# Performance work log

Hardware: AMD Instinct MI355X
Metric: run time of the kernel (lower is better)

## Reference

```python
import jax, jax.numpy as jnp
import numpy as np

P, N, M, B = 5, 30000, 50000, 256
T, C, L, ED, H, EMB, TD, NL = 13, 16, 3, 4, 128, 64, 5, 3
SRC = jnp.repeat(jnp.arange(P), P)  # edge type i = src*P + dst
DST = jnp.tile(jnp.arange(P), P)


def _affine(x, W, b):
    # x: [P, n, i], W: [P, i, o], b: [P, o]
    return jnp.einsum('pni,pio->pno', x, W) + b[:, None, :]


def _lrelu(x, s=0.01):
    return jnp.where(x >= 0, x, s * x)


def _gat(h, W, a_s, a_d, We, a_e, b, edge_index, edge_attr):
    # h: [P, N, H]; per-edge-type GATConv (heads=1, no self loops) then hetero 'max' aggregation
    hs, hd = h[SRC], h[DST]                       # [25, N, H]
    xl = jnp.einsum('enh,ehf->enf', hs, W)        # transformed source features
    xr = jnp.einsum('enh,ehf->enf', hd, W)
    als = jnp.einsum('enf,ef->en', xl, a_s)
    ald = jnp.einsum('enf,ef->en', xr, a_d)

    def per_type(xl_e, als_e, ald_e, ea, We_e, ae_e, ei):
        src, dst = ei[0], ei[1]
        alpha = als_e[src] + ald_e[dst] + (ea @ We_e) @ ae_e
        alpha = jnp.where(alpha >= 0, alpha, 0.2 * alpha)  # GAT negative_slope=0.2
        amax = jax.ops.segment_max(alpha, dst, num_segments=N)
        ex = jnp.exp(alpha - amax[dst])
        den = jax.ops.segment_sum(ex, dst, num_segments=N)
        w = ex / (den[dst] + 1e-16)
        return jax.ops.segment_sum(w[:, None] * xl_e[src], dst, num_segments=N)

    out = jax.vmap(per_type)(xl, als, ald, edge_attr, We, a_e, edge_index)
    out = out + b[:, None, :]
    return out.reshape(P, P, N, H).max(axis=0)  # HeteroConv aggr='max' over source types


def setup_inputs():
    key = jax.random.key(0)
    ks = iter(jax.random.split(key, 64))
    def nrm(shape, s=1.0):
        return jax.random.normal(next(ks), shape, dtype=jnp.float32) * s
    w = 0.05
    inp = {
        'x': nrm((P, N, T)),
        'cond_x': nrm((P, N, C + L)),
        'edge_attr': nrm((P * P, M, ED)),
        'timesteps': jax.random.uniform(next(ks), (B,), dtype=jnp.float32),
        'te1_W': nrm((1, TD), w), 'te1_b': nrm((TD,), w),
        'te2_W': nrm((TD, TD), w), 'te2_b': nrm((TD,), w),
        'emb_W': nrm((P, T + L, EMB), w), 'emb_b': nrm((P, EMB), w),
        'cemb_W': nrm((P, C, EMB), w), 'cemb_b': nrm((P, EMB), w),
        'pa_W': nrm((P, 2 * EMB, 2 * EMB), w), 'pa_b': nrm((P, 2 * EMB), w),
        'pc_W': nrm((P, 2 * EMB, EMB), w), 'pc_b': nrm((P, EMB), w),
        'sl0_W': nrm((P, EMB + TD, H), w), 'sl0_b': nrm((P, H), w),
        'sl12_W': nrm((2, P, H + TD, H), w), 'sl12_b': nrm((2, P, H), w),
        'slout_W': nrm((P, H + TD, T), w), 'slout_b': nrm((P, T), w),
        'gat_W': nrm((NL, P * P, H, H), w), 'gat_as': nrm((NL, P * P, H), w),
        'gat_ad': nrm((NL, P * P, H), w), 'gat_We': nrm((NL, P * P, ED, H), w),
        'gat_ae': nrm((NL, P * P, H), w), 'gat_b': nrm((NL, P * P, H), w),
        'xc_W': nrm((NL, P, H, H // 2), w), 'xc_b': nrm((NL, P, H // 2), w),
        'cc_W': nrm((NL, P, H, H // 2), w), 'cc_b': nrm((NL, P, H // 2), w),
        'ca_W': nrm((NL, P, H, H), w), 'ca_b': nrm((NL, P, H), w),
        'batch_idx': jax.random.randint(next(ks), (P, N), 0, B),
        'edge_index': jax.random.randint(next(ks), (P * P, 2, M), 0, N),
    }
    return inp


def reference(x, cond_x, edge_attr, timesteps, te1_W, te1_b, te2_W, te2_b,
              emb_W, emb_b, cemb_W, cemb_b, pa_W, pa_b, pc_W, pc_b,
              sl0_W, sl0_b, sl12_W, sl12_b, slout_W, slout_b,
              gat_W, gat_as, gat_ad, gat_We, gat_ae, gat_b,
              xc_W, xc_b, cc_W, cc_b, ca_W, ca_b, batch_idx, edge_index):
    # time embedding: Linear(1,TD) -> SiLU -> Linear(TD,TD)
    temb = jax.nn.silu(timesteps[:, None] @ te1_W + te1_b) @ te2_W + te2_b  # [B, TD]
    cond, latent = cond_x[..., :C], cond_x[..., C:]
    h = _affine(jnp.concatenate([x, latent], -1), emb_W, emb_b)            # [P,N,EMB]
    ce = _affine(cond, cemb_W, cemb_b)
    h = jnp.concatenate([h, ce], -1)                                       # [P,N,2EMB]
    h = jax.nn.sigmoid(_affine(h, pa_W, pa_b)) * h                         # attention pooling
    h = _affine(h, pc_W, pc_b)                                             # [P,N,EMB]
    nt = temb[batch_idx]                                                   # [P,N,TD]
    h = jnp.concatenate([h, nt], -1)
    for l in range(NL):
        if l > 0:
            h = jnp.concatenate([h, nt], -1)
        Wl, bl = (sl0_W, sl0_b) if l == 0 else (sl12_W[l - 1], sl12_b[l - 1])
        h = _lrelu(_affine(h, Wl, bl))                                     # [P,N,H]
        comm = _lrelu(_gat(h, gat_W[l], gat_as[l], gat_ad[l], gat_We[l], gat_ae[l], gat_b[l], edge_index, edge_attr))
        h = jnp.concatenate([_affine(h, xc_W[l], xc_b[l]), _affine(comm, cc_W[l], cc_b[l])], -1)
        h = h + jax.nn.sigmoid(_affine(h, ca_W[l], ca_b[l])) * h
    h = jnp.concatenate([h, nt], -1)
    return _affine(h, slout_W, slout_b)                                    # [P,N,T]
```

## Files before the change

### kernel.cpp

```cpp
#include <hip/hip_runtime.h>
#include <cstdio>

using bf8 = __attribute__((ext_vector_type(8))) short;
using f4v = __attribute__((ext_vector_type(4))) float;
typedef unsigned short u16;
typedef unsigned int u32;

#define DEV __device__ __forceinline__

DEV float bf2f(u16 u){ return __uint_as_float(((u32)u) << 16); }
DEV u16 f2bf(float f){ u32 u = __float_as_uint(f); return (u16)((u + 0x7fffu + ((u >> 16) & 1u)) >> 16); }
DEV float sigm(float v){ return 1.f / (1.f + __expf(-v)); }

constexpr int P5 = 5, NN = 30000, MM = 50000, NE = 25, BB = 256;
constexpr int KC = 96;
constexpr int RS = KC * 2 + 16;
constexpr int RSA = 272;

__global__ void temb_k(const float* ts, const float* w1, const float* b1,
                       const float* w2, const float* b2, float* temb){
  int i = blockIdx.x * blockDim.x + threadIdx.x;
  if (i >= BB) return;
  float t = ts[i]; float z[5];
#pragma unroll
  for (int j = 0; j < 5; ++j){ float u = t * w1[j] + b1[j]; z[j] = u * sigm(u); }
#pragma unroll
  for (int j2 = 0; j2 < 5; ++j2){
    float s = b2[j2];
#pragma unroll
    for (int j = 0; j < 5; ++j) s += z[j] * w2[j * 5 + j2];
    temb[i * 5 + j2] = s;
  }
}

__global__ void wtransE_k(const float* __restrict__ W, u16* __restrict__ Wt,
                          int Kreal, int Kpad, int Nreal, int Nalloc, int total){
  int idx = blockIdx.x * blockDim.x + threadIdx.x;
  if (idx >= total) return;
  int k = idx % Kpad;
  int t2 = idx / Kpad;
  int f = t2 % Nalloc;
  int b = t2 / Nalloc;
  float v = (k < Kreal && f < Nreal) ? W[((size_t)b * Kreal + k) * Nreal + f] : 0.f;
  Wt[idx] = f2bf(v);
}

__global__ void embw_k(const float* emb_W, const float* emb_b, const float* cemb_W, const float* cemb_b,
                       u16* Wc, float* bc){
  int b = blockIdx.x, f = threadIdx.x;
  for (int k = 0; k < 32; ++k){
    float v = 0.f;
    if (f < 64){ if (k < 16) v = emb_W[((size_t)b * 16 + k) * 64 + f]; }
    else       { if (k >= 16) v = cemb_W[((size_t)b * 16 + (k - 16)) * 64 + (f - 64)]; }
    Wc[((size_t)b * 128 + f) * 32 + k] = f2bf(v);
  }
  bc[b * 128 + f] = (f < 64) ? emb_b[b * 64 + f] : cemb_b[b * 64 + (f - 64)];
}

__global__ void gwtT_k(const float* __restrict__ gW, u16* __restrict__ gWt){
  int idx = blockIdx.x * blockDim.x + threadIdx.x;
  if (idx >= 75 * 128 * 128) return;
  int h = idx & 127, f = (idx >> 7) & 127, le = idx >> 14;
  gWt[idx] = f2bf(gW[(size_t)le * 16384 + h * 128 + f]);
}

__global__ void gatred_k(const float* gW, const float* gas, const float* gad,
                         const float* gWe, const float* gae,
                         float* wswd, float* eaw){
  int le = blockIdx.x; int h = threadIdx.x;
  const float* W = gW + (size_t)le * 16384;
  const float* as_ = gas + le * 128;
  const float* ad_ = gad + le * 128;
  float wsv = 0.f, wdv = 0.f;
  for (int f = 0; f < 128; ++f){
    float w = W[h * 128 + f];
    wsv += w * as_[f]; wdv += w * ad_[f];
  }
  wswd[le * 256 + h] = wsv;
  wswd[le * 256 + 128 + h] = wdv;
  if (h < 4){
    const float* We = gWe + (size_t)le * 512;
    const float* ae = gae + le * 128;
    float s = 0.f;
    for (int f = 0; f < 128; ++f) s += We[h * 128 + f] * ae[f];
    eaw[le * 4 + h] = s;
  }
}

__global__ void abuild_k(const float* x, const float* cx, u16* A0){
  int idx = blockIdx.x * blockDim.x + threadIdx.x;
  if (idx >= P5 * NN) return;
  const float* xr = x + (size_t)idx * 13;
  const float* cr = cx + (size_t)idx * 19;
  u16* a0 = A0 + (size_t)idx * 32;
#pragma unroll
  for (int i = 0; i < 13; ++i) a0[i] = f2bf(xr[i]);
#pragma unroll
  for (int i = 0; i < 3; ++i) a0[13 + i] = f2bf(cr[16 + i]);
#pragma unroll
  for (int i = 0; i < 16; ++i) a0[16 + i] = f2bf(cr[i]);
}

__global__ void ntfill_k(u16* buf, int pitch, int co, const int* bidx, const float* temb){
  int idx = blockIdx.x * blockDim.x + threadIdx.x;
  if (idx >= P5 * NN) return;
  int b = bidx[idx];
  u16* r = buf + (size_t)idx * pitch;
#pragma unroll
  for (int j = 0; j < 5; ++j) r[co + j] = f2bf(temb[b * 5 + j]);
  for (int j = co + 5; j < pitch; ++j) r[j] = 0;
}

__global__ __launch_bounds__(1024) void csr_build_k(const int* __restrict__ EI, int* __restrict__ off,
                                                    int* __restrict__ srcC, int* __restrict__ minv){
  extern __shared__ int cntl[];
  __shared__ int wsum[16];
  int e = blockIdx.x, tid = threadIdx.x;
  int lane = tid & 63, wv = tid >> 6;
  for (int i = tid; i < NN; i += 1024) cntl[i] = 0;
  __syncthreads();
  const int* srcp = EI + (size_t)e * 2 * MM;
  const int* dstp = srcp + MM;
  for (int m = tid; m < MM; m += 1024) atomicAdd(&cntl[dstp[m]], 1);
  __syncthreads();
  int t0 = tid * 30, t1 = t0 + 30;
  if (t0 > NN) t0 = NN;
  if (t1 > NN) t1 = NN;
  int tsum = 0;
  for (int i = t0; i < t1; ++i) tsum += cntl[i];
  int s = tsum;
#pragma unroll
  for (int o = 1; o < 64; o <<= 1){ int t = __shfl_up(s, o, 64); if (lane >= o) s += t; }
  if (lane == 63) wsum[wv] = s;
  __syncthreads();
  if (wv == 0 && lane < 16){
    int t = wsum[lane];
#pragma unroll
    for (int o = 1; o < 16; o <<= 1){ int u = __shfl_up(t, o, 64); if (lane >= o) t += u; }
    wsum[lane] = t;
  }
  __syncthreads();
  int run = ((wv > 0) ? wsum[wv - 1] : 0) + (s - tsum);
  for (int i = t0; i < t1; ++i){
    int v = cntl[i];
    off[(size_t)e * (NN + 1) + i] = run;
    cntl[i] = run;
    run += v;
  }
  if (tid == 0) off[(size_t)e * (NN + 1) + NN] = wsum[15];
  __syncthreads();
  for (int m = tid; m < MM; m += 1024){
    int d = dstp[m];
    int pos = atomicAdd(&cntl[d], 1);
    srcC[(size_t)e * MM + pos] = srcp[m];
    minv[(size_t)e * MM + pos] = m;
  }
}

__global__ void eadot_k(const float* __restrict__ ea, const float* __restrict__ eaw,
                        const int* __restrict__ minv, float* __restrict__ eadot){
  int idx = blockIdx.x * blockDim.x + threadIdx.x;
  if (idx >= 3 * NE * MM) return;
  int l = idx / (NE * MM);
  int rem = idx - l * NE * MM;
  int e = rem / MM, pos = rem - e * MM;
  int m = minv[(size_t)e * MM + pos];
  const float* a4 = ea + ((size_t)e * MM + m) * 4;
  const float* ew = eaw + (size_t)(l * NE + e) * 4;
  eadot[idx] = a4[0] * ew[0] + a4[1] * ew[1] + a4[2] * ew[2] + a4[3] * ew[3];
}

__global__ __launch_bounds__(256) void dots2_k(const u16* __restrict__ hS, const float* __restrict__ wswd_l,
                                               float* __restrict__ als, float* __restrict__ ald){
  __shared__ u32 hl[64][65];
  __shared__ float wsl[10][129];
  int p = blockIdx.y;
  int n0 = blockIdx.x * 64;
  int tid = threadIdx.x;
  for (int i = tid; i < 10 * 128; i += 256){
    int col = i >> 7, k = i & 127;
    int e = (col < 5) ? (p * 5 + col) : ((col - 5) * 5 + p);
    wsl[col][k] = wswd_l[e * 256 + ((col < 5) ? 0 : 128) + k];
  }
  for (int i = tid; i < 64 * 64; i += 256){
    int r = i >> 6, kp = i & 63;
    int n = n0 + r;
    hl[r][kp] = (n < NN) ? ((const u32*)hS)[((size_t)p * NN + n) * 64 + kp] : 0u;
  }
  __syncthreads();
  int col = tid & 15, rbase = tid >> 4;
  if (col < 10){
#pragma unroll
    for (int pass = 0; pass < 4; ++pass){
      int r = rbase + pass * 16;
      int n = n0 + r;
      if (n >= NN) continue;
      float s = 0.f;
#pragma unroll
      for (int kp = 0; kp < 64; ++kp){
        u32 pr = hl[r][kp];
        s += bf2f((u16)(pr & 0xffffu)) * wsl[col][2 * kp]
           + bf2f((u16)(pr >> 16)) * wsl[col][2 * kp + 1];
      }
      if (col < 5) als[(size_t)(p * 5 + col) * NN + n] = s;
      else         ald[(size_t)((col - 5) * 5 + p) * NN + n] = s;
    }
  }
}

__global__ __launch_bounds__(256) void aexp_k(const float* __restrict__ als, const float* __restrict__ ald,
                                              const float* __restrict__ eadot_l, const int* __restrict__ srcC,
                                              const int* __restrict__ off, uint2* __restrict__ prec){
  int idx = blockIdx.x * blockDim.x + threadIdx.x;
  if (idx >= NE * NN) return;
  int e = idx / NN;
  int ro = off[(size_t)e + idx], re = off[(size_t)e + idx + 1];
  if (ro >= re) return;
  float av = ald[idx];
  const int* sc = srcC + (size_t)e * MM;
  const float* ed = eadot_l + (size_t)e * MM;
  const float* ale = als + (size_t)e * NN;
  float mx = -3.0e38f;
  for (int j = ro; j < re; ++j){
    float a = ale[sc[j]] + av + ed[j];
    a = (a >= 0.f) ? a : 0.2f * a;
    mx = fmaxf(mx, a);
  }
  for (int j = ro; j < re; ++j){
    int src = sc[j];
    float a = ale[src] + av + ed[j];
    a = (a >= 0.f) ? a : 0.2f * a;
    uint2 pr; pr.x = (u32)src; pr.y = __float_as_uint(__expf(a - mx));
    prec[(size_t)e * MM + j] = pr;
  }
}

__global__ __launch_bounds__(256) void agg3_k(const u16* __restrict__ hS, const uint2* __restrict__ prec,
                                              const int* __restrict__ off, u16* __restrict__ agghB,
                                              int pd0, int npd){
  int l = threadIdx.x & 63, w = threadIdx.x >> 6;
  int n0 = blockIdx.x * 8 + w;
  int n1 = n0 + 4;
  int y = blockIdx.y;
  int ps = y / npd, e = ps * 5 + pd0 + (y - ps * npd);
  const uint2* pe = prec + (size_t)e * MM;
  const int* offe = off + (size_t)e * (NN + 1);
  const u32* hb = (const u32*)hS + (size_t)ps * NN * 64 + l;
  int ro0 = 0, ln0 = 0, ro1 = 0, ln1 = 0;
  if (n0 < NN){ ro0 = offe[n0]; ln0 = offe[n0 + 1] - ro0; }
  if (n1 < NN){ ro1 = offe[n1]; ln1 = offe[n1 + 1] - ro1; }
  float den0 = 0.f, a00 = 0.f, a01 = 0.f;
  float den1 = 0.f, a10 = 0.f, a11 = 0.f;
  int mx = (ln0 > ln1) ? ln0 : ln1;
  for (int t = 0; t < mx; ++t){
    if (t < ln0){
      uint2 pr = pe[ro0 + t];
      float ex = __uint_as_float(pr.y);
      u32 hv = hb[(size_t)pr.x * 64];
      den0 += ex; a00 += ex * bf2f((u16)(hv & 0xffffu)); a01 += ex * bf2f((u16)(hv >> 16));
    }
    if (t < ln1){
      uint2 pr = pe[ro1 + t];
      float ex = __uint_as_float(pr.y);
      u32 hv = hb[(size_t)pr.x * 64];
      den1 += ex; a10 += ex * bf2f((u16)(hv & 0xffffu)); a11 += ex * bf2f((u16)(hv >> 16));
    }
  }
  if (n0 < NN){
    float inv = 1.f / (den0 + 1e-16f);
    ((u32*)agghB)[((size_t)y * NN + n0) * 64 + l] = (u32)f2bf(a00 * inv) | ((u32)f2bf(a01 * inv) << 16);
  }
  if (n1 < NN){
    float inv = 1.f / (den1 + 1e-16f);
    ((u32*)agghB)[((size_t)y * NN + n1) * 64 + l] = (u32)f2bf(a10 * inv) | ((u32)f2bf(a11 * inv) << 16);
  }
}

template<int NF, int MI, int NJ, int EPI, bool ALRELU>
__global__ __launch_bounds__(256) void tgemm_k(const u16* __restrict__ A, const u16* __restrict__ Wt,
                                               const float* __restrict__ bias, void* __restrict__ out,
                                               const u16* __restrict__ X,
                                               int Kpad, int opitch, int ocol, int xpitch){
  constexpr int Nalloc = NF * 16;
  constexpr int WR = 128 / (MI * 16);
  constexpr int WC = 4 / WR;
  static_assert(WR * WC == 4 && NJ * WC * 16 == Nalloc, "wave tiling");
  extern __shared__ __align__(16) char smem[];
  float* Cs = (float*)smem;
  const int tid = threadIdx.x;
  const int l = tid & 63, w = tid >> 6;
  const int bz = blockIdx.z;
  const int r0 = blockIdx.x * 128;
  const int wr = w / WC, wc = w % WC;
  const size_t Ab = (size_t)bz * NN;

  f4v acc[MI][NJ];
#pragma unroll
  for (int i = 0; i < MI; ++i)
#pragma unroll
    for (int j = 0; j < NJ; ++j) acc[i][j] = f4v{0.f, 0.f, 0.f, 0.f};

  for (int kb = 0; kb < Kpad; kb += KC){
    int kc = Kpad - kb; if (kc > KC) kc = KC;
    int nseg = kc >> 3;
    for (int s = tid; s < 128 * nseg; s += 256){
      int r = s / nseg, c = s - r * nseg;
      int grow = r0 + r; if (grow > NN - 1) grow = NN - 1;
      uint4 v = *(const uint4*)(A + (Ab + grow) * Kpad + kb + c * 8);
      if (ALRELU){
        u32 pr[4] = {v.x, v.y, v.z, v.w};
#pragma unroll
        for (int q = 0; q < 4; ++q){
          float lo = bf2f((u16)(pr[q] & 0xffffu)), hi = bf2f((u16)(pr[q] >> 16));
          lo = lo >= 0.f ? lo : 0.01f * lo; hi = hi >= 0.f ? hi : 0.01f * hi;
          pr[q] = (u32)f2bf(lo) | ((u32)f2bf(hi) << 16);
        }
        v.x = pr[0]; v.y = pr[1]; v.z = pr[2]; v.w = pr[3];
      }
      *(uint4*)(smem + r * RS + c * 16) = v;
    }
    for (int s = tid; s < Nalloc * nseg; s += 256){
      int r = s / nseg, c = s - r * nseg;
      uint4 v = *(const uint4*)(Wt + ((size_t)bz * Nalloc + r) * Kpad + kb + c * 8);
      *(uint4*)(smem + 128 * RS + r * RS + c * 16) = v;
    }
    __syncthreads();
    int KI = kc >> 5;
    for (int k0 = 0; k0 < KI; ++k0){
      bf8 af[MI], bfr[NJ];
#pragma unroll
      for (int i = 0; i < MI; ++i){
        int row = wr * (MI * 16) + i * 16 + (l & 15);
        af[i] = *(const bf8*)(smem + row * RS + k0 * 64 + (l >> 4) * 16);
      }
#pragma unroll
      for (int j = 0; j < NJ; ++j){
        int col = wc * (NJ * 16) + j * 16 + (l & 15);
        bfr[j] = *(const bf8*)(smem + 128 * RS + col * RS + k0 * 64 + (l >> 4) * 16);
      }
#pragma unroll
      for (int i = 0; i < MI; ++i)
#pragma unroll
        for (int j = 0; j < NJ; ++j)
          acc[i][j] = __builtin_amdgcn_mfma_f32_16x16x32_bf16(af[i], bfr[j], acc[i][j], 0, 0, 0);
    }
    __syncthreads();
  }

  if (EPI == 4){
    int col = l & 15;
    if (col < 13){
#pragma unroll
      for (int i = 0; i < MI; ++i){
        float bv = bias[bz * 13 + col];
#pragma unroll
        for (int r = 0; r < 4; ++r){
          int grow = r0 + wr * (MI * 16) + i * 16 + (l >> 4) * 4 + r;
          if (grow < NN)
            ((float*)out)[((size_t)bz * NN + grow) * 13 + col] = acc[i][0][r] + bv;
        }
      }
    }
    return;
  }

#pragma unroll
  for (int i = 0; i < MI; ++i)
#pragma unroll
    for (int j = 0; j < NJ; ++j){
      int tcol = wc * (NJ * 16) + j * 16 + (l & 15);
      float bv = bias[bz * Nalloc + tcol];
#pragma unroll
      for (int r = 0; r < 4; ++r){
        int trow = wr * (MI * 16) + i * 16 + (l >> 4) * 4 + r;
        float v = acc[i][j][r] + bv;
        if (EPI == 2) v = v >= 0.f ? v : 0.01f * v;
        Cs[trow * Nalloc + tcol] = v;
      }
    }
  __syncthreads();
  constexpr int nsc = Nalloc / 4;
  u16* o16 = (u16*)out;
  for (int s = tid; s < 128 * nsc; s += 256){
    int r = s / nsc, c = s - r * nsc;
    int grow = r0 + r; if (grow >= NN) continue;
    float4 cv = *(const float4*)(Cs + r * Nalloc + c * 4);
    float v0 = cv.x, v1 = cv.y, v2 = cv.z, v3 = cv.w;
    if (EPI == 1){
      uint2 xv = *(const uint2*)(X + ((size_t)bz * NN + grow) * xpitch + c * 4);
      float x0 = bf2f((u16)(xv.x & 0xffffu)), x1 = bf2f((u16)(xv.x >> 16));
      float x2 = bf2f((u16)(xv.y & 0xffffu)), x3 = bf2f((u16)(xv.y >> 16));
      v0 = x0 * sigm(v0); v1 = x1 * sigm(v1); v2 = x2 * sigm(v2); v3 = x3 * sigm(v3);
    }
    uint2 ov;
    ov.x = (u32)f2bf(v0) | ((u32)f2bf(v1) << 16);
    ov.y = (u32)f2bf(v2) | ((u32)f2bf(v3) << 16);
    *(uint2*)(o16 + ((size_t)bz * NN + grow) * opitch + ocol + c * 4) = ov;
  }
}

__global__ __launch_bounds__(256) void tgatmm_k(const u16* __restrict__ agghB, const u16* __restrict__ gWt_l,
                                                const float* __restrict__ gb_l, u16* __restrict__ comm,
                                                int pd){
  extern __shared__ __align__(16) char smem[];
  char* As = smem;
  char* Bs = smem + 64 * RSA;
  float* Cs = (float*)smem;
  const int tid = threadIdx.x, l = tid & 63, w = tid >> 6;
  const int r0 = blockIdx.x * 64;
  const int wr = w >> 1, wc = w & 1;
  f4v vmax[2][4];
#pragma unroll 1
  for (int ps = 0; ps < 5; ++ps){
    int e = ps * 5 + pd;
    const u16* aggs = agghB + (size_t)ps * NN * 128;
    const u16* wb = gWt_l + (size_t)e * 16384;
    for (int s = tid; s < 64 * 16; s += 256){
      int r = s >> 4, c = s & 15;
      int grow = r0 + r; if (grow > NN - 1) grow = NN - 1;
      *(uint4*)(As + r * RSA + c * 16) = *(const uint4*)(aggs + (size_t)grow * 128 + c * 8);
    }
    for (int s = tid; s < 128 * 16; s += 256){
      int r = s >> 4, c = s & 15;
      *(uint4*)(Bs + r * RSA + c * 16) = *(const uint4*)(wb + r * 128 + c * 8);
    }
    __syncthreads();
    f4v acc[2][4];
#pragma unroll
    for (int i = 0; i < 2; ++i)
#pragma unroll
      for (int j = 0; j < 4; ++j) acc[i][j] = f4v{0.f, 0.f, 0.f, 0.f};
#pragma unroll
    for (int k0 = 0; k0 < 4; ++k0){
      bf8 af[2], bfr[4];
#pragma unroll
      for (int i = 0; i < 2; ++i)
        af[i] = *(const bf8*)(As + (wr * 32 + i * 16 + (l & 15)) * RSA + k0 * 64 + (l >> 4) * 16);
#pragma unroll
      for (int j = 0; j < 4; ++j)
        bfr[j] = *(const bf8*)(Bs + (wc * 64 + j * 16 + (l & 15)) * RSA + k0 * 64 + (l >> 4) * 16);
#pragma unroll
      for (int i = 0; i < 2; ++i)
#pragma unroll
        for (int j = 0; j < 4; ++j)
          acc[i][j] = __builtin_amdgcn_mfma_f32_16x16x32_bf16(af[i], bfr[j], acc[i][j], 0, 0, 0);
    }
    const float* be = gb_l + e * 128;
#pragma unroll
    for (int i = 0; i < 2; ++i)
#pragma unroll
      for (int j = 0; j < 4; ++j){
        int tcol = wc * 64 + j * 16 + (l & 15);
        float bv = be[tcol];
#pragma unroll
        for (int r = 0; r < 4; ++r){
          float cvv = acc[i][j][r] + bv;
          vmax[i][j][r] = (ps == 0) ? cvv : fmaxf(vmax[i][j][r], cvv);
        }
      }
    __syncthreads();
  }
#pragma unroll
  for (int i = 0; i < 2; ++i)
#pragma unroll
    for (int j = 0; j < 4; ++j){
      int tcol = wc * 64 + j * 16 + (l & 15);
#pragma unroll
      for (int r = 0; r < 4; ++r){
        int trow = wr * 32 + i * 16 + (l >> 4) * 4 + r;
        Cs[trow * 128 + tcol] = vmax[i][j][r];
      }
    }
  __syncthreads();
  for (int s = tid; s < 64 * 32; s += 256){
    int r = s >> 5, c = s & 31;
    int grow = r0 + r; if (grow >= NN) continue;
    float4 cv = *(const float4*)(Cs + r * 128 + c * 4);
    uint2 ov;
    ov.x = (u32)f2bf(cv.x) | ((u32)f2bf(cv.y) << 16);
    ov.y = (u32)f2bf(cv.z) | ((u32)f2bf(cv.w) << 16);
    *(uint2*)(comm + ((size_t)pd * NN + grow) * 128 + c * 4) = ov;
  }
}

__global__ __launch_bounds__(512) void fca_k(const u16* __restrict__ hS, const u16* __restrict__ comm,
                                             const u16* __restrict__ wxc_l, const float* __restrict__ bxc_l,
                                             const u16* __restrict__ wcc_l, const float* __restrict__ bcc_l,
                                             const u16* __restrict__ wca_l, const float* __restrict__ bca_l,
                                             const int* __restrict__ bidx, const float* __restrict__ temb,
                                             u16* __restrict__ hL){
  extern __shared__ __align__(16) char smem[];
  char* As = smem;
  char* H2 = smem + 128 * RSA;
  const int tid = threadIdx.x, l = tid & 63, wv = tid >> 6;
  const int wr = wv >> 1, wc = wv & 1;
  const int bz = blockIdx.z;
  const int r0 = blockIdx.x * 128;
  const size_t pb = (size_t)bz * NN;

  f4v acc_a[2][2], acc_b[2][2];
  for (int s = tid; s < 128 * 16; s += 512){
    int r = s >> 4, c = s & 15;
    int grow = r0 + r; if (grow > NN - 1) grow = NN - 1;
    *(uint4*)(As + r * RSA + c * 16) = *(const uint4*)(hS + (pb + grow) * 128 + c * 8);
  }
  for (int s = tid; s < 64 * 16; s += 512){
    int r = s >> 4, c = s & 15;
    *(uint4*)(H2 + r * RSA + c * 16) = *(const uint4*)(wxc_l + (size_t)bz * 8192 + r * 128 + c * 8);
  }
  __syncthreads();
#pragma unroll
  for (int i = 0; i < 2; ++i)
#pragma unroll
    for (int j = 0; j < 2; ++j) acc_a[i][j] = f4v{0.f, 0.f, 0.f, 0.f};
#pragma unroll
  for (int k0 = 0; k0 < 4; ++k0){
    bf8 af[2], bfr[2];
#pragma unroll
    for (int i = 0; i < 2; ++i)
      af[i] = *(const bf8*)(As + (wr * 32 + i * 16 + (l & 15)) * RSA + k0 * 64 + (l >> 4) * 16);
#pragma unroll
    for (int j = 0; j < 2; ++j)
      bfr[j] = *(const bf8*)(H2 + (wc * 32 + j * 16 + (l & 15)) * RSA + k0 * 64 + (l >> 4) * 16);
#pragma unroll
    for (int i = 0; i < 2; ++i)
#pragma unroll
      for (int j = 0; j < 2; ++j)
        acc_a[i][j] = __builtin_amdgcn_mfma_f32_16x16x32_bf16(af[i], bfr[j], acc_a[i][j], 0, 0, 0);
  }
  __syncthreads();
  for (int s = tid; s < 128 * 16; s += 512){
    int r = s >> 4, c = s & 15;
    int grow = r0 + r; if (grow > NN - 1) grow = NN - 1;
    uint4 v = *(const uint4*)(comm + (pb + grow) * 128 + c * 8);
    u32 pr[4] = {v.x, v.y, v.z, v.w};
#pragma unroll
    for (int q = 0; q < 4; ++q){
      float lo = bf2f((u16)(pr[q] & 0xffffu)), hi = bf2f((u16)(pr[q] >> 16));
      lo = lo >= 0.f ? lo : 0.01f * lo; hi = hi >= 0.f ? hi : 0.01f * hi;
      pr[q] = (u32)f2bf(lo) | ((u32)f2bf(hi) << 16);
    }
    v.x = pr[0]; v.y = pr[1]; v.z = pr[2]; v.w = pr[3];
    *(uint4*)(As + r * RSA + c * 16) = v;
  }
  for (int s = tid; s < 64 * 16; s += 512){
    int r = s >> 4, c = s & 15;
    *(uint4*)(H2 + r * RSA + c * 16) = *(const uint4*)(wcc_l + (size_t)bz * 8192 + r * 128 + c * 8);
  }
  __syncthreads();
#pragma unroll
  for (int i = 0; i < 2; ++i)
#pragma unroll
    for (int j = 0; j < 2; ++j) acc_b[i][j] = f4v{0.f, 0.f, 0.f, 0.f};
#pragma unroll
  for (int k0 = 0; k0 < 4; ++k0){
    bf8 af[2], bfr[2];
#pragma unroll
    for (int i = 0; i < 2; ++i)
      af[i] = *(const bf8*)(As + (wr * 32 + i * 16 + (l & 15)) * RSA + k0 * 64 + (l >> 4) * 16);
#pragma unroll
    for (int j = 0; j < 2; ++j)
      bfr[j] = *(const bf8*)(H2 + (wc * 32 + j * 16 + (l & 15)) * RSA + k0 * 64 + (l >> 4) * 16);
#pragma unroll
    for (int i = 0; i < 2; ++i)
#pragma unroll
      for (int j = 0; j < 2; ++j)
        acc_b[i][j] = __builtin_amdgcn_mfma_f32_16x16x32_bf16(af[i], bfr[j], acc_b[i][j], 0, 0, 0);
  }
  __syncthreads();
#pragma unroll
  for (int i = 0; i < 2; ++i)
#pragma unroll
    for (int j = 0; j < 2; ++j){
      int colL = wc * 32 + j * 16 + (l & 15);
      float bL = bxc_l[bz * 64 + colL];
      float bR = bcc_l[bz * 64 + colL];
#pragma unroll
      for (int r = 0; r < 4; ++r){
        int row = wr * 32 + i * 16 + (l >> 4) * 4 + r;
        *(u16*)(H2 + row * RSA + colL * 2)        = f2bf(acc_a[i][j][r] + bL);
        *(u16*)(H2 + row * RSA + (colL + 64) * 2) = f2bf(acc_b[i][j][r] + bR);
      }
    }
  for (int s = tid; s < 128 * 16; s += 512){
    int r = s >> 4, c = s & 15;
    *(uint4*)(As + r * RSA + c * 16) = *(const uint4*)(wca_l + (size_t)bz * 16384 + r * 128 + c * 8);
  }
  __syncthreads();
  f4v acc_g[2][4];
#pragma unroll
  for (int i = 0; i < 2; ++i)
#pragma unroll
    for (int j = 0; j < 4; ++j) acc_g[i][j] = f4v{0.f, 0.f, 0.f, 0.f};
#pragma unroll
  for (int k0 = 0; k0 < 4; ++k0){
    bf8 af[2], bfr[4];
#pragma unroll
    for (int i = 0; i < 2; ++i)
      af[i] = *(const bf8*)(H2 + (wr * 32 + i * 16 + (l & 15)) * RSA + k0 * 64 + (l >> 4) * 16);
#pragma unroll
    for (int j = 0; j < 4; ++j)
      bfr[j] = *(const bf8*)(As + (wc * 64 + j * 16 + (l & 15)) * RSA + k0 * 64 + (l >> 4) * 16);
#pragma unroll
    for (int i = 0; i < 2; ++i)
#pragma unroll
      for (int j = 0; j < 4; ++j)
        acc_g[i][j] = __builtin_amdgcn_mfma_f32_16x16x32_bf16(af[i], bfr[j], acc_g[i][j], 0, 0, 0);
  }
  float vout[2][4][4];
#pragma unroll
  for (int i = 0; i < 2; ++i)
#pragma unroll
    for (int j = 0; j < 4; ++j){
      int col = wc * 64 + j * 16 + (l & 15);
      float bv = bca_l[bz * 128 + col];
#pragma unroll
      for (int r = 0; r < 4; ++r){
        int row = wr * 32 + i * 16 + (l >> 4) * 4 + r;
        float xg = bf2f(*(const u16*)(H2 + row * RSA + col * 2));
        vout[i][j][r] = xg * (1.f + sigm(acc_g[i][j][r] + bv));
      }
    }
  __syncthreads();
#pragma unroll
  for (int i = 0; i < 2; ++i)
#pragma unroll
    for (int j = 0; j < 4; ++j){
      int col = wc * 64 + j * 16 + (l & 15);
#pragma unroll
      for (int r = 0; r < 4; ++r){
        int row = wr * 32 + i * 16 + (l >> 4) * 4 + r;
        *(u16*)(H2 + row * RSA + col * 2) = f2bf(vout[i][j][r]);
      }
    }
  __syncthreads();
  for (int s = tid; s < 128 * 40; s += 512){
    int r = s / 40, c = s - r * 40;
    int grow = r0 + r; if (grow >= NN) continue;
    if (c < 32){
      uint2 v = *(const uint2*)(H2 + r * RSA + c * 8);
      *(uint2*)(hL + (pb + grow) * 160 + c * 4) = v;
    } else {
      int b = bidx[pb + grow];
      int col0 = c * 4;
      u16 t[4];
#pragma unroll
      for (int q = 0; q < 4; ++q){
        int j = col0 + q - 128;
        t[q] = (j < 5) ? f2bf(temb[b * 5 + j]) : (u16)0;
      }
      uint2 ov;
      ov.x = (u32)t[0] | ((u32)t[1] << 16);
      ov.y = (u32)t[2] | ((u32)t[3] << 16);
      *(uint2*)(hL + (pb + grow) * 160 + col0) = ov;
    }
  }
}

constexpr size_t ALN(size_t x){ return (x + 255) & ~(size_t)255; }
constexpr size_t SZ_A0   = ALN((size_t)P5 * NN * 32 * 2);
constexpr size_t SZ_H0   = ALN((size_t)P5 * NN * 96 * 2);
constexpr size_t SZ_H128 = ALN((size_t)P5 * NN * 128 * 2);
constexpr size_t SZ_HL   = ALN((size_t)P5 * NN * 160 * 2);
constexpr size_t O_A0 = 0;
constexpr size_t O_H0 = O_A0 + SZ_A0;
constexpr size_t O_AGG = 0;
constexpr size_t O_HCAT = O_H0 + SZ_H0;
constexpr size_t O_HG = O_HCAT + SZ_H128;
constexpr size_t O_HS = O_HG + SZ_H128;
constexpr size_t O_HL = O_HS + SZ_H128;
constexpr size_t O_TEMB = O_HL + SZ_HL;
constexpr size_t O_WSWD = O_TEMB + ALN(256 * 5 * 4);
constexpr size_t O_EAW  = O_WSWD + ALN(75 * 256 * 4);
constexpr size_t O_OFFS = O_EAW + ALN(75 * 4 * 4);
constexpr size_t O_ALS  = O_OFFS + ALN((size_t)NE * (NN + 1) * 4);
constexpr size_t O_ALD  = O_ALS + ALN((size_t)NE * NN * 4);
constexpr size_t O_SRCC = O_ALD + ALN((size_t)NE * NN * 4);
constexpr size_t O_MINV = O_SRCC + ALN((size_t)NE * MM * 4);
constexpr size_t O_EADOT= O_MINV + ALN((size_t)NE * MM * 4);
constexpr size_t O_GWT  = O_EADOT + ALN((size_t)3 * NE * MM * 4);
constexpr size_t O_WCMB = O_GWT + ALN((size_t)75 * 16384 * 2);
constexpr size_t O_BCMB = O_WCMB + ALN((size_t)5 * 128 * 32 * 2);
constexpr size_t O_WPA  = O_BCMB + ALN((size_t)5 * 128 * 4);
constexpr size_t O_WPC  = O_WPA + ALN((size_t)5 * 128 * 128 * 2);
constexpr size_t O_WSL0 = O_WPC + ALN((size_t)5 * 64 * 128 * 2);
constexpr size_t O_WSL12= O_WSL0 + ALN((size_t)5 * 128 * 96 * 2);
constexpr size_t O_WSLO = O_WSL12 + ALN((size_t)10 * 128 * 160 * 2);
constexpr size_t O_WXC  = O_WSLO + ALN((size_t)5 * 16 * 160 * 2);
constexpr size_t O_WCC  = O_WXC + ALN((size_t)15 * 64 * 128 * 2);
constexpr size_t O_WCA  = O_WCC + ALN((size_t)15 * 64 * 128 * 2);
constexpr size_t O_PREC = O_WCA + ALN((size_t)15 * 128 * 128 * 2);
constexpr size_t WS_NEED= O_PREC + ALN((size_t)NE * MM * 8);

extern "C" void kernel_launch(void* const* d_in, const int* in_sizes, int n_in,
                              void* d_out, int out_size, void* d_ws, size_t ws_size,
                              hipStream_t stream){
  if (ws_size < WS_NEED){
    fprintf(stderr, "kernel_launch: ws too small: need %zu have %zu\n", WS_NEED, ws_size);
    return;
  }
  const float* x        = (const float*)d_in[0];
  const float* cond_x   = (const float*)d_in[1];
  const float* edge_attr= (const float*)d_in[2];
  const float* timesteps= (const float*)d_in[3];
  const float* te1_W = (const float*)d_in[4];
  const float* te1_b = (const float*)d_in[5];
  const float* te2_W = (const float*)d_in[6];
  const float* te2_b = (const float*)d_in[7];
  const float* emb_W = (const float*)d_in[8];
  const float* emb_b = (const float*)d_in[9];
  const float* cemb_W= (const float*)d_in[10];
  const float* cemb_b= (const float*)d_in[11];
  const float* pa_W  = (const float*)d_in[12];
  const float* pa_b  = (const float*)d_in[13];
  const float* pc_W  = (const float*)d_in[14];
  const float* pc_b  = (const float*)d_in[15];
  const float* sl0_W = (const float*)d_in[16];
  const float* sl0_b = (const float*)d_in[17];
  const float* sl12_W= (const float*)d_in[18];
  const float* sl12_b= (const float*)d_in[19];
  const float* slout_W=(const float*)d_in[20];
  const float* slout_b=(const float*)d_in[21];
  const float* gat_W = (const float*)d_in[22];
  const float* gat_as= (const float*)d_in[23];
  const float* gat_ad= (const float*)d_in[24];
  const float* gat_We= (const float*)d_in[25];
  const float* gat_ae= (const float*)d_in[26];
  const float* gat_b = (const float*)d_in[27];
  const float* xc_W  = (const float*)d_in[28];
  const float* xc_b  = (const float*)d_in[29];
  const float* cc_W  = (const float*)d_in[30];
  const float* cc_b  = (const float*)d_in[31];
  const float* ca_W  = (const float*)d_in[32];
  const float* ca_b  = (const float*)d_in[33];
  const int* batch_idx = (const int*)d_in[34];
  const int* edge_index= (const int*)d_in[35];

  char* ws = (char*)d_ws;
  u16* A0    = (u16*)(ws + O_A0);
  u16* h0buf = (u16*)(ws + O_H0);
  u16* agghB = (u16*)(ws + O_AGG);
  u16* hcat  = (u16*)(ws + O_HCAT);
  u16* hg    = (u16*)(ws + O_HG);
  u16* comm  = (u16*)(ws + O_HG);
  u16* hS    = (u16*)(ws + O_HS);
  u16* hL    = (u16*)(ws + O_HL);
  float* tembp = (float*)(ws + O_TEMB);
  float* wswdp = (float*)(ws + O_WSWD);
  float* eawp  = (float*)(ws + O_EAW);
  int* offs = (int*)(ws + O_OFFS);
  float* alsp = (float*)(ws + O_ALS);
  float* aldp = (float*)(ws + O_ALD);
  int* srcCp = (int*)(ws + O_SRCC);
  int* minvp = (int*)(ws + O_MINV);
  float* eadotp = (float*)(ws + O_EADOT);
  u16* gwt   = (u16*)(ws + O_GWT);
  u16* wcmb  = (u16*)(ws + O_WCMB);
  float* bcmb= (float*)(ws + O_BCMB);
  u16* wpa   = (u16*)(ws + O_WPA);
  u16* wpc   = (u16*)(ws + O_WPC);
  u16* wsl0  = (u16*)(ws + O_WSL0);
  u16* wsl12 = (u16*)(ws + O_WSL12);
  u16* wslo  = (u16*)(ws + O_WSLO);
  u16* wxc   = (u16*)(ws + O_WXC);
  u16* wcc   = (u16*)(ws + O_WCC);
  u16* wca   = (u16*)(ws + O_WCA);
  uint2* precp = (uint2*)(ws + O_PREC);

  const dim3 B256(256);
  const dim3 TG(235, 1, 5);
  const int GPN = (P5 * NN + 255) / 256;
  const int GEN = (NE * NN + 255) / 256;
  constexpr int LDS_N128 = 65536;
  constexpr int LDS_N64  = 39936;
  constexpr int LDS_SLO  = 29952;
  constexpr int LDS_TGAT = 64 * RSA + 128 * RSA;
  constexpr int LDS_FCA  = 128 * RSA * 2;
  constexpr int LDS_CSR  = NN * 4;

  temb_k<<<1, B256, 0, stream>>>(timesteps, te1_W, te1_b, te2_W, te2_b, tembp);
  embw_k<<<5, 128, 0, stream>>>(emb_W, emb_b, cemb_W, cemb_b, wcmb, bcmb);
  {
    auto WT = [&](const float* W, u16* Wt, int Kr, int Kp, int Nr, int Na, int B){
      int total = B * Na * Kp;
      wtransE_k<<<(total + 255) / 256, B256, 0, stream>>>(W, Wt, Kr, Kp, Nr, Na, total);
    };
    WT(pa_W, wpa, 128, 128, 128, 128, 5);
    WT(pc_W, wpc, 128, 128, 64, 64, 5);
    WT(sl0_W, wsl0, 69, 96, 128, 128, 5);
    WT(sl12_W, wsl12, 133, 160, 128, 128, 10);
    WT(slout_W, wslo, 133, 160, 13, 16, 5);
    WT(xc_W, wxc, 128, 128, 64, 64, 15);
    WT(cc_W, wcc, 128, 128, 64, 64, 15);
    WT(ca_W, wca, 128, 128, 128, 128, 15);
  }
  gwtT_k<<<(75 * 128 * 128 + 255) / 256, B256, 0, stream>>>(gat_W, gwt);
  gatred_k<<<75, 128, 0, stream>>>(gat_W, gat_as, gat_ad, gat_We, gat_ae, wswdp, eawp);

  csr_build_k<<<25, 1024, LDS_CSR, stream>>>(edge_index, offs, srcCp, minvp);
  eadot_k<<<(3 * NE * MM + 255) / 256, B256, 0, stream>>>(edge_attr, eawp, minvp, eadotp);

  abuild_k<<<GPN, B256, 0, stream>>>(x, cond_x, A0);
  tgemm_k<8, 4, 4, 0, false><<<TG, B256, LDS_N128, stream>>>(A0, wcmb, bcmb, hcat, nullptr, 32, 128, 0, 0);
  tgemm_k<8, 4, 4, 1, false><<<TG, B256, LDS_N128, stream>>>(hcat, wpa, pa_b, hg, hcat, 128, 128, 0, 128);
  tgemm_k<4, 2, 4, 0, false><<<TG, B256, LDS_N64, stream>>>(hg, wpc, pc_b, h0buf, nullptr, 128, 96, 0, 0);
  ntfill_k<<<GPN, B256, 0, stream>>>(h0buf, 96, 64, batch_idx, tembp);

  for (int l = 0; l < 3; ++l){
    if (l == 0)
      tgemm_k<8, 4, 4, 2, false><<<TG, B256, LDS_N128, stream>>>(h0buf, wsl0, sl0_b, hS, nullptr, 96, 128, 0, 0);
    else
      tgemm_k<8, 4, 4, 2, false><<<TG, B256, LDS_N128, stream>>>(hL, wsl12 + (size_t)(l - 1) * 5 * 128 * 160,
                                                                 sl12_b + (size_t)(l - 1) * 5 * 128, hS, nullptr,
                                                                 160, 128, 0, 0);
    const float* wswd_l = wswdp + (size_t)l * 25 * 256;
    const u16* gwt_l = gwt + (size_t)l * 25 * 16384;
    const float* gb_l = gat_b + (size_t)l * 25 * 128;
    dots2_k<<<dim3(469, 5), B256, 0, stream>>>(hS, wswd_l, alsp, aldp);
    aexp_k<<<GEN, B256, 0, stream>>>(alsp, aldp, eadotp + (size_t)l * NE * MM, srcCp, offs, precp);
    for (int pd = 0; pd < 5; ++pd){
      agg3_k<<<dim3(3750, 5), B256, 0, stream>>>(hS, precp, offs, agghB, pd, 1);
      tgatmm_k<<<dim3(469), B256, LDS_TGAT, stream>>>(agghB, gwt_l, gb_l, comm, pd);
    }
    fca_k<<<dim3(235, 1, 5), 512, LDS_FCA, stream>>>(hS, comm,
        wxc + (size_t)l * 5 * 64 * 128, xc_b + (size_t)l * 5 * 64,
        wcc + (size_t)l * 5 * 64 * 128, cc_b + (size_t)l * 5 * 64,
        wca + (size_t)l * 5 * 128 * 128, ca_b + (size_t)l * 5 * 128,
        batch_idx, tembp, hL);
  }

  tgemm_k<1, 2, 1, 4, false><<<TG, B256, LDS_SLO, stream>>>(hL, wslo, slout_b, d_out, nullptr, 160, 13, 0, 0);
}
```

Baseline: 1.914 ms.

## Parallelize CSR build across edge segments with multi-kernel histogram scan

Replaces the single-block-per-edge-type CSR build (25 blocks) with a segmented pipeline: per-segment histograms across 250 blocks, a two-level prefix scan, and a parallel fill that uses per-segment base offsets. Source index and original edge index are packed into one int2 array, so the fill writes once and the consumers read once. The aim is to remove the serial bottleneck of 25 large blocks doing atomics and a scan over 50k edges. It adds several extra launches and scratch buffers that reuse early workspace, and the order of edges within each destination now depends on atomic ordering per segment.

Result: faster. 1.803 ms (-5.8%).

```diff
diff --git a/kernel.cpp b/kernel.cpp
--- a/kernel.cpp
+++ b/kernel.cpp
@@ -16,6 +16,7 @@
 constexpr int KC = 96;
 constexpr int RS = KC * 2 + 16;
 constexpr int RSA = 272;
+constexpr int NSEG = 10, SEG = MM / NSEG;
 
 __global__ void temb_k(const float* ts, const float* w1, const float* b1,
                        const float* w2, const float* b2, float* temb){
@@ -111,60 +112,118 @@
   for (int j = co + 5; j < pitch; ++j) r[j] = 0;
 }
 
-__global__ __launch_bounds__(1024) void csr_build_k(const int* __restrict__ EI, int* __restrict__ off,
-                                                    int* __restrict__ srcC, int* __restrict__ minv){
+__global__ __launch_bounds__(1024) void csr_cnt_k(const int* __restrict__ EI, u16* __restrict__ hseg){
   extern __shared__ int cntl[];
+  int b = blockIdx.x; int e = b / NSEG, s = b - e * NSEG;
+  int tid = threadIdx.x;
+  for (int i = tid; i < NN; i += 1024) cntl[i] = 0;
+  __syncthreads();
+  const int* dstp = EI + (size_t)e * 2 * MM + MM;
+  int m0 = s * SEG;
+  for (int m = m0 + tid; m < m0 + SEG; m += 1024) atomicAdd(&cntl[dstp[m]], 1);
+  __syncthreads();
+  u16* hp = hseg + ((size_t)e * NSEG + s) * NN;
+  for (int i = tid; i < NN; i += 1024) hp[i] = (u16)cntl[i];
+}
+
+__global__ __launch_bounds__(1024) void csr_b1_k(const u16* __restrict__ hseg, int* __restrict__ ctot){
+  __shared__ int red[16];
+  int e = blockIdx.x / 30, c = blockIdx.x % 30;
+  int tid = threadIdx.x, lane = tid & 63;
+  int d = c * 1000 + tid;
+  int tot = 0;
+  if (tid < 1000 && d < NN){
+    const u16* hb = hseg + (size_t)e * NSEG * NN + d;
+    for (int s = 0; s < NSEG; ++s) tot += hb[(size_t)s * NN];
+  }
+  int v = tot;
+#pragma unroll
+  for (int o = 32; o > 0; o >>= 1) v += __shfl_down(v, o, 64);
+  if (lane == 0) red[tid >> 6] = v;
+  __syncthreads();
+  if (tid == 0){
+    int u = 0;
+#pragma unroll
+    for (int i = 0; i < 16; ++i) u += red[i];
+    ctot[e * 30 + c] = u;
+  }
+}
+
+__global__ void csr_b2_k(const int* __restrict__ ctot, int* __restrict__ cbase, int* __restrict__ off){
+  int e = blockIdx.x, lane = threadIdx.x;
+  int v = (lane < 30) ? ctot[e * 30 + lane] : 0;
+  int s = v;
+#pragma unroll
+  for (int o = 1; o < 32; o <<= 1){ int t = __shfl_up(s, o, 64); if (lane >= o) s += t; }
+  if (lane < 30) cbase[e * 30 + lane] = s - v;
+  if (lane == 29) off[(size_t)e * (NN + 1) + NN] = s;
+}
+
+__global__ __launch_bounds__(1024) void csr_b3_k(const u16* __restrict__ hseg, const int* __restrict__ cbase,
+                                                 int* __restrict__ off, u32* __restrict__ bseg){
   __shared__ int wsum[16];
-  int e = blockIdx.x, tid = threadIdx.x;
-  int lane = tid & 63, wv = tid >> 6;
-  for (int i = tid; i < NN; i += 1024) cntl[i] = 0;
+  int e = blockIdx.x / 30, c = blockIdx.x % 30;
+  int tid = threadIdx.x, lane = tid & 63, wv = tid >> 6;
+  int d = c * 1000 + tid;
+  bool ok = (tid < 1000 && d < NN);
+  int h[NSEG]; int tot = 0;
+  if (ok){
+    const u16* hb = hseg + (size_t)e * NSEG * NN + d;
+#pragma unroll
+    for (int s = 0; s < NSEG; ++s){ h[s] = hb[(size_t)s * NN]; tot += h[s]; }
+  } else {
+#pragma unroll
+    for (int s = 0; s < NSEG; ++s) h[s] = 0;
+  }
+  int v = tot, s1 = v;
+#pragma unroll
+  for (int o = 1; o < 64; o <<= 1){ int t = __shfl_up(s1, o, 64); if (lane >= o) s1 += t; }
+  if (lane == 63) wsum[wv] = s1;
+  __syncthreads();
+  if (wv == 0 && lane < 16){
+    int t = wsum[lane];
+#pragma unroll
+    for (int o = 1; o < 16; o <<= 1){ int u = __shfl_up(t, o, 64); if (lane >= o) t += u; }
+    wsum[lane] = t;
+  }
+  __syncthreads();
+  int excl = ((wv > 0) ? wsum[wv - 1] : 0) + (s1 - v) + cbase[e * 30 + c];
+  if (ok){
+    off[(size_t)e * (NN + 1) + d] = excl;
+    u32 b = (u32)excl;
+    u32* bb = bseg + (size_t)e * NSEG * NN + d;
+#pragma unroll
+    for (int s = 0; s < NSEG; ++s){ bb[(size_t)s * NN] = b; b += (u32)h[s]; }
+  }
+}
+
+__global__ __launch_bounds__(1024) void csr_fill_k(const int* __restrict__ EI, const u32* __restrict__ bseg,
+                                                   int2* __restrict__ sm){
+  extern __shared__ int cntl[];
+  int b = blockIdx.x; int e = b / NSEG, s = b - e * NSEG;
+  int tid = threadIdx.x;
+  const u32* bp = bseg + ((size_t)e * NSEG + s) * NN;
+  for (int i = tid; i < NN; i += 1024) cntl[i] = (int)bp[i];
   __syncthreads();
   const int* srcp = EI + (size_t)e * 2 * MM;
   const int* dstp = srcp + MM;
-  for (int m = tid; m < MM; m += 1024) atomicAdd(&cntl[dstp[m]], 1);
-  __syncthreads();
-  int t0 = tid * 30, t1 = t0 + 30;
-  if (t0 > NN) t0 = NN;
-  if (t1 > NN) t1 = NN;
-  int tsum = 0;
-  for (int i = t0; i < t1; ++i) tsum += cntl[i];
-  int s = tsum;
-#pragma unroll
-  for (int o = 1; o < 64; o <<= 1){ int t = __shfl_up(s, o, 64); if (lane >= o) s += t; }
-  if (lane == 63) wsum[wv] = s;
-  __syncthreads();
-  if (wv == 0 && lane < 16){
-    int t = wsum[lane];
-#pragma unroll
-    for (int o = 1; o < 16; o <<= 1){ int u = __shfl_up(t, o, 64); if (lane >= o) t += u; }
-    wsum[lane] = t;
-  }
-  __syncthreads();
-  int run = ((wv > 0) ? wsum[wv - 1] : 0) + (s - tsum);
-  for (int i = t0; i < t1; ++i){
-    int v = cntl[i];
-    off[(size_t)e * (NN + 1) + i] = run;
-    cntl[i] = run;
-    run += v;
-  }
-  if (tid == 0) off[(size_t)e * (NN + 1) + NN] = wsum[15];
-  __syncthreads();
-  for (int m = tid; m < MM; m += 1024){
+  int m0 = s * SEG;
+  for (int m = m0 + tid; m < m0 + SEG; m += 1024){
     int d = dstp[m];
     int pos = atomicAdd(&cntl[d], 1);
-    srcC[(size_t)e * MM + pos] = srcp[m];
-    minv[(size_t)e * MM + pos] = m;
+    int2 v; v.x = srcp[m]; v.y = m;
+    sm[(size_t)e * MM + pos] = v;
   }
 }
 
 __global__ void eadot_k(const float* __restrict__ ea, const float* __restrict__ eaw,
-                        const int* __restrict__ minv, float* __restrict__ eadot){
+                        const int2* __restrict__ sm, float* __restrict__ eadot){
   int idx = blockIdx.x * blockDim.x + threadIdx.x;
   if (idx >= 3 * NE * MM) return;
   int l = idx / (NE * MM);
   int rem = idx - l * NE * MM;
   int e = rem / MM, pos = rem - e * MM;
-  int m = minv[(size_t)e * MM + pos];
+  int m = sm[(size_t)e * MM + pos].y;
   const float* a4 = ea + ((size_t)e * MM + m) * 4;
   const float* ew = eaw + (size_t)(l * NE + e) * 4;
   eadot[idx] = a4[0] * ew[0] + a4[1] * ew[1] + a4[2] * ew[2] + a4[3] * ew[3];
@@ -209,7 +268,7 @@
 }
 
 __global__ __launch_bounds__(256) void aexp_k(const float* __restrict__ als, const float* __restrict__ ald,
-                                              const float* __restrict__ eadot_l, const int* __restrict__ srcC,
+                                              const float* __restrict__ eadot_l, const int2* __restrict__ sm,
                                               const int* __restrict__ off, uint2* __restrict__ prec){
   int idx = blockIdx.x * blockDim.x + threadIdx.x;
   if (idx >= NE * NN) return;
@@ -217,17 +276,17 @@
   int ro = off[(size_t)e + idx], re = off[(size_t)e + idx + 1];
   if (ro >= re) return;
   float av = ald[idx];
-  const int* sc = srcC + (size_t)e * MM;
+  const int2* sc = sm + (size_t)e * MM;
   const float* ed = eadot_l + (size_t)e * MM;
   const float* ale = als + (size_t)e * NN;
   float mx = -3.0e38f;
   for (int j = ro; j < re; ++j){
-    float a = ale[sc[j]] + av + ed[j];
+    float a = ale[sc[j].x] + av + ed[j];
     a = (a >= 0.f) ? a : 0.2f * a;
     mx = fmaxf(mx, a);
   }
   for (int j = ro; j < re; ++j){
-    int src = sc[j];
+    int src = sc[j].x;
     float a = ale[src] + av + ed[j];
     a = (a >= 0.f) ? a : 0.2f * a;
     uint2 pr; pr.x = (u32)src; pr.y = __float_as_uint(__expf(a - mx));
@@ -669,15 +728,18 @@
 constexpr size_t O_HG = O_HCAT + SZ_H128;
 constexpr size_t O_HS = O_HG + SZ_H128;
 constexpr size_t O_HL = O_HS + SZ_H128;
+constexpr size_t O_HSEG = 0;
+constexpr size_t O_BSEG = O_HSEG + ALN((size_t)NE * NSEG * NN * 2);
+constexpr size_t O_CTOT = O_BSEG + ALN((size_t)NE * NSEG * NN * 4);
+constexpr size_t O_CBASE= O_CTOT + ALN((size_t)NE * 30 * 4);
 constexpr size_t O_TEMB = O_HL + SZ_HL;
 constexpr size_t O_WSWD = O_TEMB + ALN(256 * 5 * 4);
 constexpr size_t O_EAW  = O_WSWD + ALN(75 * 256 * 4);
 constexpr size_t O_OFFS = O_EAW + ALN(75 * 4 * 4);
 constexpr size_t O_ALS  = O_OFFS + ALN((size_t)NE * (NN + 1) * 4);
 constexpr size_t O_ALD  = O_ALS + ALN((size_t)NE * NN * 4);
-constexpr size_t O_SRCC = O_ALD + ALN((size_t)NE * NN * 4);
-constexpr size_t O_MINV = O_SRCC + ALN((size_t)NE * MM * 4);
-constexpr size_t O_EADOT= O_MINV + ALN((size_t)NE * MM * 4);
+constexpr size_t O_SM   = O_ALD + ALN((size_t)NE * NN * 4);
+constexpr size_t O_EADOT= O_SM + ALN((size_t)NE * MM * 8);
 constexpr size_t O_GWT  = O_EADOT + ALN((size_t)3 * NE * MM * 4);
 constexpr size_t O_WCMB = O_GWT + ALN((size_t)75 * 16384 * 2);
 constexpr size_t O_BCMB = O_WCMB + ALN((size_t)5 * 128 * 32 * 2);
@@ -745,14 +807,17 @@
   u16* comm  = (u16*)(ws + O_HG);
   u16* hS    = (u16*)(ws + O_HS);
   u16* hL    = (u16*)(ws + O_HL);
+  u16* hseg  = (u16*)(ws + O_HSEG);
+  u32* bseg  = (u32*)(ws + O_BSEG);
+  int* ctot  = (int*)(ws + O_CTOT);
+  int* cbase = (int*)(ws + O_CBASE);
   float* tembp = (float*)(ws + O_TEMB);
   float* wswdp = (float*)(ws + O_WSWD);
   float* eawp  = (float*)(ws + O_EAW);
   int* offs = (int*)(ws + O_OFFS);
   float* alsp = (float*)(ws + O_ALS);
   float* aldp = (float*)(ws + O_ALD);
-  int* srcCp = (int*)(ws + O_SRCC);
-  int* minvp = (int*)(ws + O_MINV);
+  int2* smp  = (int2*)(ws + O_SM);
   float* eadotp = (float*)(ws + O_EADOT);
   u16* gwt   = (u16*)(ws + O_GWT);
   u16* wcmb  = (u16*)(ws + O_WCMB);
@@ -797,8 +862,12 @@
   gwtT_k<<<(75 * 128 * 128 + 255) / 256, B256, 0, stream>>>(gat_W, gwt);
   gatred_k<<<75, 128, 0, stream>>>(gat_W, gat_as, gat_ad, gat_We, gat_ae, wswdp, eawp);
 
-  csr_build_k<<<25, 1024, LDS_CSR, stream>>>(edge_index, offs, srcCp, minvp);
-  eadot_k<<<(3 * NE * MM + 255) / 256, B256, 0, stream>>>(edge_attr, eawp, minvp, eadotp);
+  csr_cnt_k<<<NE * NSEG, 1024, LDS_CSR, stream>>>(edge_index, hseg);
+  csr_b1_k<<<NE * 30, 1024, 0, stream>>>(hseg, ctot);
+  csr_b2_k<<<NE, 64, 0, stream>>>(ctot, cbase, offs);
+  csr_b3_k<<<NE * 30, 1024, 0, stream>>>(hseg, cbase, offs, bseg);
+  csr_fill_k<<<NE * NSEG, 1024, LDS_CSR, stream>>>(edge_index, bseg, smp);
+  eadot_k<<<(3 * NE * MM + 255) / 256, B256, 0, stream>>>(edge_attr, eawp, smp, eadotp);
 
   abuild_k<<<GPN, B256, 0, stream>>>(x, cond_x, A0);
   tgemm_k<8, 4, 4, 0, false><<<TG, B256, LDS_N128, stream>>>(A0, wcmb, bcmb, hcat, nullptr, 32, 128, 0, 0);
@@ -817,7 +886,7 @@
     const u16* gwt_l = gwt + (size_t)l * 25 * 16384;
     const float* gb_l = gat_b + (size_t)l * 25 * 128;
     dots2_k<<<dim3(469, 5), B256, 0, stream>>>(hS, wswd_l, alsp, aldp);
-    aexp_k<<<GEN, B256, 0, stream>>>(alsp, aldp, eadotp + (size_t)l * NE * MM, srcCp, offs, precp);
+    aexp_k<<<GEN, B256, 0, stream>>>(alsp, aldp, eadotp + (size_t)l * NE * MM, smp, offs, precp);
     for (int pd = 0; pd < 5; ++pd){
       agg3_k<<<dim3(3750, 5), B256, 0, stream>>>(hS, precp, offs, agghB, pd, 1);
       tgatmm_k<<<dim3(469), B256, LDS_TGAT, stream>>>(agghB, gwt_l, gb_l, comm, pd);
```
